# Performance work log

Measured on AMD Instinct MI355X. Metric: run time of the kernel, lower is better.

Reference implementation:

```python
import jax, jax.numpy as jnp
import numpy as np

N = 16384      # total nodes in batched graph
E = 131072     # message-passing edges
E_RO = 32768   # readout edges
D = 1024       # fc7 appearance feature dim
DL = 300       # word2vec dim
DS = 16        # spatial edge feature dim
C = 117        # HICO verb classes


def setup_inputs() -> dict:
    key = jax.random.key(0)
    ks = jax.random.split(key, 20)
    s = 0.02
    return {
        'feat': jax.random.normal(ks[0], (N, D), jnp.float32),
        'word2vec': jax.random.normal(ks[1], (N, DL), jnp.float32),
        's_f': jax.random.normal(ks[2], (E, DS), jnp.float32),
        's_f_ro': jax.random.normal(ks[3], (E_RO, DS), jnp.float32),
        'W_e': jax.random.normal(ks[4], (2 * D + DS, D), jnp.float32) * s,
        'b_e': jnp.zeros((D,), jnp.float32),
        'W_el': jax.random.normal(ks[5], (2 * DL, DL), jnp.float32) * s,
        'b_el': jnp.zeros((DL,), jnp.float32),
        'W_nu': jax.random.normal(ks[6], (2 * D, D), jnp.float32) * s,
        'b_nu': jnp.zeros((D,), jnp.float32),
        'W_nul': jax.random.normal(ks[7], (2 * DL, DL), jnp.float32) * s,
        'b_nul': jnp.zeros((DL,), jnp.float32),
        'W_p': jax.random.normal(ks[8], (D + DL + DS + DL + D, C), jnp.float32) * s,
        'b_p': jnp.zeros((C,), jnp.float32),
        'edge_src': jax.random.randint(ks[9], (E,), 0, N, jnp.int32),
        'edge_dst': jax.random.randint(ks[10], (E,), 0, N, jnp.int32),
        'ro_src': jax.random.randint(ks[11], (E_RO,), 0, N, jnp.int32),
        'ro_dst': jax.random.randint(ks[12], (E_RO,), 0, N, jnp.int32),
    }


def _mean_agg(msgs, dst, n, dtype):
    # scatter-add messages to destination nodes, then mean-normalize
    summed = jax.ops.segment_sum(msgs, dst, num_segments=n)
    cnt = jax.ops.segment_sum(jnp.ones((msgs.shape[0], 1), dtype), dst, num_segments=n)
    return summed / jnp.maximum(cnt, 1.0)


def reference(feat, word2vec, s_f, s_f_ro, W_e, b_e, W_el, b_el,
              W_nu, b_nu, W_nul, b_nul, W_p, b_p,
              edge_src, edge_dst, ro_src, ro_dst):
    # --- GRNN message passing: gather -> concat -> MLP -> scatter(mean) ---
    # appearance stream: [src_feat, dst_feat, s_f] -> relu(MLP)
    m = jax.nn.relu(
        jnp.concatenate([feat[edge_src], feat[edge_dst], s_f], axis=1) @ W_e + b_e)
    agg = _mean_agg(m, edge_dst, N, feat.dtype)               # [N, D]
    # language stream: [src_w2v, dst_w2v] -> relu(MLP)
    ml = jax.nn.relu(
        jnp.concatenate([word2vec[edge_src], word2vec[edge_dst]], axis=1) @ W_el + b_el)
    aggl = _mean_agg(ml, edge_dst, N, feat.dtype)             # [N, DL]

    # --- NodeUpdate: concat(original, aggregated) -> MLP ---
    new_n_f = jax.nn.relu(jnp.concatenate([feat, agg], axis=1) @ W_nu + b_nu)
    new_n_f_lang = jax.nn.relu(
        jnp.concatenate([word2vec, aggl], axis=1) @ W_nul + b_nul)

    # --- Predictor (edge readout): concat[dst_f, dst_lang, s_f, src_lang, src_f] ---
    ef = jnp.concatenate([
        new_n_f[ro_dst], new_n_f_lang[ro_dst], s_f_ro,
        new_n_f_lang[ro_src], new_n_f[ro_src]], axis=1)       # [E_RO, 2664]
    pred = ef @ W_p + b_p                                     # [E_RO, 117]
    return pred
```

## Files before the change

### kernel.cpp

```cpp
#include <hip/hip_runtime.h>

typedef unsigned short u16;
typedef __attribute__((ext_vector_type(8))) short short8;
typedef __attribute__((ext_vector_type(4))) float f32x4;

#define NN 16384
#define EE 131072
#define ERO 32768
#define DF 1024
#define DL 300
#define DLP 320
#define DLN 384
#define DS 16
#define NC 117
#define NCP 128

__device__ __forceinline__ float bf2f(u16 x) {
  unsigned int u = ((unsigned int)x) << 16;
  float f;
  __builtin_memcpy(&f, &u, 4);
  return f;
}
__device__ __forceinline__ u16 f2bf(float f) {
  unsigned int u;
  __builtin_memcpy(&u, &f, 4);
  u = (u + 0x7FFFu + ((u >> 16) & 1u)) >> 16;
  return (u16)u;
}
__device__ __forceinline__ float ld1(const void* p, size_t i, int f) {
  return f ? ((const float*)p)[i] : bf2f(((const u16*)p)[i]);
}
__device__ __forceinline__ void ld4(const void* p, size_t i, int f,
                                    float& x, float& y, float& z, float& w) {
  if (f) {
    float4 v = *(const float4*)((const float*)p + i);
    x = v.x; y = v.y; z = v.z; w = v.w;
  } else {
    ushort4 v = *(const ushort4*)((const u16*)p + i);
    x = bf2f(v.x); y = bf2f(v.y); z = bf2f(v.z); w = bf2f(v.w);
  }
}
__device__ __forceinline__ const void* eoff(const void* p, size_t off, int f) {
  return f ? (const void*)((const float*)p + off) : (const void*)((const u16*)p + off);
}

__global__ void detect_kernel(const unsigned int* __restrict__ w, int* __restrict__ flag) {
  unsigned int x = w[threadIdx.x];
  int e = (x >> 7) & 0xFF;
  int ok = (e >= 97 && e <= 157);
  unsigned long long m = __ballot(ok);
  if (threadIdx.x == 0) flag[0] = (__popcll(m) >= 48) ? 0 : 1;
}

__global__ void cast_bf16(const int* __restrict__ flag, const void* __restrict__ src,
                          u16* __restrict__ dst, int total8) {
  const int i = blockIdx.x * 256 + threadIdx.x;
  if (i >= total8) return;
  const int fin = flag[0];
  const size_t o = (size_t)i * 8;
  float x0, x1, x2, x3, x4, x5, x6, x7;
  ld4(src, o, fin, x0, x1, x2, x3);
  ld4(src, o + 4, fin, x4, x5, x6, x7);
  ushort4 lo, hi;
  lo.x = f2bf(x0); lo.y = f2bf(x1); lo.z = f2bf(x2); lo.w = f2bf(x3);
  hi.x = f2bf(x4); hi.y = f2bf(x5); hi.z = f2bf(x6); hi.w = f2bf(x7);
  *(ushort4*)(dst + o) = lo;
  *(ushort4*)(dst + o + 4) = hi;
}

struct TJob {
  const void* W; long off;
  int Kr, Nr, Nstr, Kp, Np, blk0;
};
struct TPack { TJob j[12]; int nj; };

__global__ void prep_weights(const int* __restrict__ flag, TPack P, u16* __restrict__ outbase,
                             const long* __restrict__ outoffs_unused) {
}

struct TJob2 {
  const void* W; long off;
  u16* out;
  int Kr, Nr, Nstr, Kp, Np, blk0;
};
struct TPack2 { TJob2 j[12]; int nj; };

__global__ void prep_weights2(const int* __restrict__ flag, TPack2 P) {
  int b = blockIdx.x;
  int ji = 0;
  while (ji + 1 < P.nj && b >= P.j[ji + 1].blk0) ++ji;
  const TJob2 J = P.j[ji];
  const int idx = (b - J.blk0) * 256 + threadIdx.x;
  if (idx >= J.Np * J.Kp) return;
  const int n = idx / J.Kp, k = idx % J.Kp;
  float v = 0.f;
  if (k < J.Kr && n < J.Nr) v = ld1(J.W, (size_t)J.off + (size_t)k * J.Nstr + n, flag[0]);
  J.out[idx] = f2bf(v);
}

__device__ __forceinline__ void stage_bf16_async(const u16* __restrict__ G, size_t rbase,
                                                 int lda, int k0, u16* lds, int w, int lane) {
  #pragma unroll
  for (int t = 0; t < 2; ++t) {
    const int rr = (w << 5) + (t << 4) + (lane >> 2);
    const u16* gp = G + (rbase + rr) * (size_t)lda + k0 + ((lane & 3) << 3);
    __builtin_amdgcn_global_load_lds(
        (const __attribute__((address_space(1))) void*)gp,
        (__attribute__((address_space(3))) void*)(lds + (((w << 5) + (t << 4)) * 32)),
        16, 0, 0);
  }
}

__device__ __forceinline__ void stage_f32_manual(const float* __restrict__ G, int row0,
                                                 int lda, int k0, int Kreal,
                                                 u16* lds, int tid) {
  const int r = tid >> 1, half = tid & 1;
  const float* gp = G + (size_t)(row0 + r) * lda + k0 + (half << 4);
  #pragma unroll
  for (int qq = 0; qq < 4; ++qq) {
    const int kk = k0 + (half << 4) + (qq << 2);
    float4 v = make_float4(0.f, 0.f, 0.f, 0.f);
    if (kk < Kreal) v = *(const float4*)(gp + (qq << 2));
    ushort4 o;
    o.x = f2bf(v.x); o.y = f2bf(v.y); o.z = f2bf(v.z); o.w = f2bf(v.w);
    *(ushort4*)(lds + r * 32 + (half << 4) + (qq << 2)) = o;
  }
}

__device__ __forceinline__ void kloop(int am, const void* __restrict__ A, int lda,
                                      int Kreal, int Kpad, const u16* __restrict__ B,
                                      u16* As, u16* Bs, f32x4 (&acc)[4][4],
                                      int row0, int col0,
                                      int tid, int lane, int w, int wm, int wn, int ml, int q) {
  for (int k0 = 0; k0 < Kpad; k0 += 32) {
    if (am == 0) stage_bf16_async((const u16*)A, (size_t)row0, lda, k0, As, w, lane);
    else         stage_f32_manual((const float*)A, row0, lda, k0, Kreal, As, tid);
    stage_bf16_async(B, (size_t)col0, Kpad, k0, Bs, w, lane);
    __syncthreads();
    short8 af[4], bfr[4];
    #pragma unroll
    for (int i = 0; i < 4; ++i)
      af[i] = *(const short8*)(As + ((wm << 6) + (i << 4) + ml) * 32 + (q << 3));
    #pragma unroll
    for (int j = 0; j < 4; ++j)
      bfr[j] = *(const short8*)(Bs + ((wn << 6) + (j << 4) + ml) * 32 + (q << 3));
    #pragma unroll
    for (int i = 0; i < 4; ++i)
      #pragma unroll
      for (int j = 0; j < 4; ++j)
        acc[i][j] = __builtin_amdgcn_mfma_f32_16x16x32_bf16(af[i], bfr[j], acc[i][j], 0, 0, 0);
    __syncthreads();
  }
}

struct GJob {
  const void* A1; const u16* B1;
  const void* A2; const u16* B2;
  const void* bias; void* C;
  int lda1, K1real, K1pad, am1;
  int lda2, K2real, K2pad, am2;
  int inBias, ldc, Nreal, Npad, relu, cf32;
  int gx, gy, blk0;
};
struct GPack { GJob j[2]; int nj; };

__global__ __launch_bounds__(256) void mfma_jobs(const int* __restrict__ flag, GPack P) {
  const int b = blockIdx.x;
  int ji = 0;
  if (P.nj > 1 && b >= P.j[1].blk0) ji = 1;
  const GJob J = P.j[ji];
  const int t = b - J.blk0;
  const int xcd = t & 7, s = t >> 3;
  const int row_t = xcd * (J.gy >> 3) + s / J.gx;
  const int col_t = s % J.gx;
  const int row0 = row_t << 7;
  const int col0 = col_t << 7;

  __shared__ __attribute__((aligned(16))) u16 As[128 * 32];
  __shared__ __attribute__((aligned(16))) u16 Bs[128 * 32];
  const int tid = threadIdx.x;
  const int lane = tid & 63;
  const int w = tid >> 6;
  const int wm = w >> 1, wn = w & 1;
  const int ml = lane & 15, q = lane >> 4;

  f32x4 acc[4][4];
  #pragma unroll
  for (int i = 0; i < 4; ++i)
    #pragma unroll
    for (int j = 0; j < 4; ++j) {
      f32x4 z = {0.f, 0.f, 0.f, 0.f};
      acc[i][j] = z;
    }

  kloop(J.am1, J.A1, J.lda1, J.K1real, J.K1pad, J.B1, As, Bs, acc,
        row0, col0, tid, lane, w, wm, wn, ml, q);
  if (J.am2 >= 0)
    kloop(J.am2, J.A2, J.lda2, J.K2real, J.K2pad, J.B2, As, Bs, acc,
          row0, col0, tid, lane, w, wm, wn, ml, q);

  const int fin = flag[0];
  #pragma unroll
  for (int j = 0; j < 4; ++j) {
    const int col = col0 + (wn << 6) + (j << 4) + ml;
    if (col >= J.Npad) continue;
    float bv = 0.f;
    if (J.bias && col < J.Nreal) bv = ld1(J.bias, col, J.inBias ? fin : 0);
    #pragma unroll
    for (int i = 0; i < 4; ++i) {
      #pragma unroll
      for (int r = 0; r < 4; ++r) {
        const int row = row0 + (wm << 6) + (i << 4) + (q << 2) + r;
        float v = 0.f;
        if (col < J.Nreal) {
          v = acc[i][j][r] + bv;
          if (J.relu) v = fmaxf(v, 0.f);
        }
        if (J.cf32) ((float*)J.C)[(size_t)row * J.ldc + col] = v;
        else        ((u16*)J.C)[(size_t)row * J.ldc + col] = f2bf(v);
      }
    }
  }
}

__global__ void cnt_kernel(const int* __restrict__ edst, int* __restrict__ cnt) {
  const int i = blockIdx.x * 256 + threadIdx.x;
  if (i < EE) atomicAdd(&cnt[edst[i]], 1);
}

__global__ __launch_bounds__(1024) void scan_kernel(const int* __restrict__ cnt,
                                                    int* __restrict__ offs,
                                                    int* __restrict__ woffs) {
  __shared__ int part[1024];
  const int t = threadIdx.x;
  const int base = t * 16;
  int loc[16];
  int s = 0;
  #pragma unroll
  for (int i = 0; i < 16; ++i) { loc[i] = s; s += cnt[base + i]; }
  part[t] = s;
  __syncthreads();
  for (int off = 1; off < 1024; off <<= 1) {
    int v = (t >= off) ? part[t - off] : 0;
    __syncthreads();
    part[t] += v;
    __syncthreads();
  }
  const int chunk_excl = (t == 0) ? 0 : part[t - 1];
  #pragma unroll
  for (int i = 0; i < 16; ++i) {
    int o = chunk_excl + loc[i];
    offs[base + i] = o;
    woffs[base + i] = o;
  }
  if (t == 1023) offs[NN] = part[1023];
}

__global__ void scatter_kernel(const int* __restrict__ esrc, const int* __restrict__ edst,
                               int* __restrict__ woffs,
                               int* __restrict__ order, int* __restrict__ srcs) {
  const int e = blockIdx.x * 256 + threadIdx.x;
  if (e < EE) {
    const int d = edst[e];
    const int pos = atomicAdd(&woffs[d], 1);
    order[pos] = e;
    srcs[pos] = esrc[e];
  }
}

__global__ __launch_bounds__(256) void app_agg(
    const int* __restrict__ flag,
    const u16* __restrict__ P12, const void* __restrict__ s_f,
    const void* __restrict__ W_eb, const void* __restrict__ b_e,
    const int* __restrict__ offs, const int* __restrict__ order,
    const int* __restrict__ srcs, u16* __restrict__ aggn)
{
  const int fin = flag[0];
  const int n = blockIdx.x;
  const int tid = threadIdx.x;
  const int c4 = tid << 2;
  const void* W_es = eoff(W_eb, (size_t)2 * DF * DF, fin);

  float wx[16], wy[16], wz[16], ww[16];
  #pragma unroll
  for (int k = 0; k < 16; ++k)
    ld4(W_es, (size_t)k * DF + c4, fin, wx[k], wy[k], wz[k], ww[k]);

  float be0, be1, be2, be3;
  ld4(b_e, c4, fin, be0, be1, be2, be3);
  const ushort4 p2 = *(const ushort4*)(P12 + (size_t)n * 2048 + 1024 + c4);
  const float base0 = bf2f(p2.x) + be0;
  const float base1 = bf2f(p2.y) + be1;
  const float base2 = bf2f(p2.z) + be2;
  const float base3 = bf2f(p2.w) + be3;

  const int beg = offs[n], end = offs[n + 1];
  float a0 = 0.f, a1 = 0.f, a2 = 0.f, a3 = 0.f;
  int j = beg;
  for (; j + 4 <= end; j += 4) {
    int ee[4], ss[4];
    #pragma unroll
    for (int m = 0; m < 4; ++m) { ee[m] = order[j + m]; ss[m] = srcs[j + m]; }
    float u0[4], u1[4], u2[4], u3[4], sfv[4][16];
    #pragma unroll
    for (int m = 0; m < 4; ++m) {
      #pragma unroll
      for (int k = 0; k < 16; k += 4)
        ld4(s_f, (size_t)ee[m] * DS + k, fin,
            sfv[m][k], sfv[m][k + 1], sfv[m][k + 2], sfv[m][k + 3]);
      const ushort4 pm = *(const ushort4*)(P12 + (size_t)ss[m] * 2048 + c4);
      u0[m] = bf2f(pm.x) + base0;
      u1[m] = bf2f(pm.y) + base1;
      u2[m] = bf2f(pm.z) + base2;
      u3[m] = bf2f(pm.w) + base3;
    }
    #pragma unroll
    for (int k = 0; k < 16; ++k)
      #pragma unroll
      for (int m = 0; m < 4; ++m) {
        u0[m] = fmaf(sfv[m][k], wx[k], u0[m]);
        u1[m] = fmaf(sfv[m][k], wy[k], u1[m]);
        u2[m] = fmaf(sfv[m][k], wz[k], u2[m]);
        u3[m] = fmaf(sfv[m][k], ww[k], u3[m]);
      }
    #pragma unroll
    for (int m = 0; m < 4; ++m) {
      a0 += fmaxf(u0[m], 0.f); a1 += fmaxf(u1[m], 0.f);
      a2 += fmaxf(u2[m], 0.f); a3 += fmaxf(u3[m], 0.f);
    }
  }
  for (; j < end; ++j) {
    const int e = order[j], s = srcs[j];
    float sf[16];
    #pragma unroll
    for (int k = 0; k < 16; k += 4)
      ld4(s_f, (size_t)e * DS + k, fin, sf[k], sf[k + 1], sf[k + 2], sf[k + 3]);
    const ushort4 p1 = *(const ushort4*)(P12 + (size_t)s * 2048 + c4);
    float v0 = bf2f(p1.x) + base0;
    float v1 = bf2f(p1.y) + base1;
    float v2 = bf2f(p1.z) + base2;
    float v3 = bf2f(p1.w) + base3;
    #pragma unroll
    for (int k = 0; k < 16; ++k) {
      v0 = fmaf(sf[k], wx[k], v0);
      v1 = fmaf(sf[k], wy[k], v1);
      v2 = fmaf(sf[k], wz[k], v2);
      v3 = fmaf(sf[k], ww[k], v3);
    }
    a0 += fmaxf(v0, 0.f); a1 += fmaxf(v1, 0.f);
    a2 += fmaxf(v2, 0.f); a3 += fmaxf(v3, 0.f);
  }
  const float inv = 1.f / fmaxf((float)(end - beg), 1.f);
  ushort4 o;
  o.x = f2bf(a0 * inv); o.y = f2bf(a1 * inv);
  o.z = f2bf(a2 * inv); o.w = f2bf(a3 * inv);
  *(ushort4*)(aggn + (size_t)n * DF + c4) = o;
}

__global__ __launch_bounds__(320) void lang_agg(
    const int* __restrict__ flag,
    const u16* __restrict__ Q12, const void* __restrict__ b_el,
    const int* __restrict__ offs, const int* __restrict__ srcs,
    u16* __restrict__ aggln)
{
  const int fin = flag[0];
  const int n = blockIdx.x;
  const int c = threadIdx.x;
  if (c >= DL) { aggln[(size_t)n * DLP + c] = 0; return; }
  const float base = bf2f(Q12[(size_t)n * 768 + 384 + c]) + ld1(b_el, c, fin);
  const int beg = offs[n], end = offs[n + 1];
  float s0 = 0.f, s1 = 0.f, s2 = 0.f, s3 = 0.f;
  int j = beg;
  for (; j + 4 <= end; j += 4) {
    s0 += fmaxf(bf2f(Q12[(size_t)srcs[j] * 768 + c]) + base, 0.f);
    s1 += fmaxf(bf2f(Q12[(size_t)srcs[j + 1] * 768 + c]) + base, 0.f);
    s2 += fmaxf(bf2f(Q12[(size_t)srcs[j + 2] * 768 + c]) + base, 0.f);
    s3 += fmaxf(bf2f(Q12[(size_t)srcs[j + 3] * 768 + c]) + base, 0.f);
  }
  for (; j < end; ++j) s0 += fmaxf(bf2f(Q12[(size_t)srcs[j] * 768 + c]) + base, 0.f);
  const float a = (s0 + s1) + (s2 + s3);
  aggln[(size_t)n * DLP + c] = f2bf(a / fmaxf((float)(end - beg), 1.f));
}

__global__ __launch_bounds__(256) void readout_kernel(
    const int* __restrict__ flag,
    const float* __restrict__ RdRs,
    const void* __restrict__ s_f_ro,
    const void* __restrict__ W_pb, size_t offWps,
    const void* __restrict__ b_p,
    const int* __restrict__ rsrc, const int* __restrict__ rdst, void* __restrict__ out)
{
  const int fin = flag[0];
  __shared__ float wps[16 * NC];
  const void* Wp_s = eoff(W_pb, offWps, fin);
  const int tid = threadIdx.x;
  for (int i = tid; i < 16 * NC; i += 256) wps[i] = ld1(Wp_s, i, fin);
  __syncthreads();
  const int slot = tid >> 7;
  const int c = tid & 127;
  const float bp = (c < NC) ? ld1(b_p, c, fin) : 0.f;

  const int e0 = (blockIdx.x << 3) + slot;
  #pragma unroll
  for (int ee = 0; ee < 8; ee += 2) {
    const int e = e0 + ee;
    const int s = rsrc[e];
    const int d = rdst[e];
    if (c < NC) {
      float acc = RdRs[(size_t)d * 256 + c] + RdRs[(size_t)s * 256 + 128 + c] + bp;
      #pragma unroll
      for (int k = 0; k < 16; ++k)
        acc = fmaf(ld1(s_f_ro, (size_t)e * DS + k, fin), wps[k * NC + c], acc);
      if (fin) ((float*)out)[(size_t)e * NC + c] = acc;
      else     ((u16*)out)[(size_t)e * NC + c] = f2bf(acc);
    }
  }
}

extern "C" void kernel_launch(void* const* d_in, const int* in_sizes, int n_in,
                              void* d_out, int out_size, void* d_ws, size_t ws_size,
                              hipStream_t stream)
{
  const void* feat  = d_in[0];
  const void* w2v   = d_in[1];
  const void* s_f   = d_in[2];
  const void* s_fro = d_in[3];
  const void* W_e   = d_in[4];
  const void* b_e   = d_in[5];
  const void* W_el  = d_in[6];
  const void* b_el  = d_in[7];
  const void* W_nu  = d_in[8];
  const void* b_nu  = d_in[9];
  const void* W_nul = d_in[10];
  const void* b_nul = d_in[11];
  const void* W_p   = d_in[12];
  const void* b_p   = d_in[13];
  const int* esrc  = (const int*)d_in[14];
  const int* edst  = (const int*)d_in[15];
  const int* rsrc  = (const int*)d_in[16];
  const int* rdst  = (const int*)d_in[17];

  char* p = (char*)d_ws;
  int* flag  = (int*)p; p += 256;
  int* cnt   = (int*)p; p += (size_t)NN * 4;
  int* offs  = (int*)p; p += (size_t)(NN + 64) * 4;
  int* woffs = (int*)p; p += (size_t)NN * 4;
  int* order = (int*)p; p += (size_t)EE * 4;
  int* srcs  = (int*)p; p += (size_t)EE * 4;
  u16* featB  = (u16*)p; p += (size_t)NN * DF * 2;
  u16* We12T  = (u16*)p; p += (size_t)2 * DF * DF * 2;
  u16* Wnu1T  = (u16*)p; p += (size_t)DF * DF * 2;
  u16* Wnu2T  = (u16*)p; p += (size_t)DF * DF * 2;
  u16* Wel12T = (u16*)p; p += (size_t)2 * DLN * DLP * 2;
  u16* Wnul1T = (u16*)p; p += (size_t)DLN * DLP * 2;
  u16* Wnul2T = (u16*)p; p += (size_t)DLN * DLP * 2;
  u16* WpFT2  = (u16*)p; p += (size_t)2 * NCP * DF * 2;
  u16* WpLT2  = (u16*)p; p += (size_t)2 * NCP * DLP * 2;
  u16* P12   = (u16*)p; p += (size_t)NN * 2048 * 2;
  u16* Q12   = (u16*)p; p += (size_t)NN * 768 * 2;
  u16* aggln = (u16*)p; p += (size_t)NN * DLP * 2;
  u16* aggn  = (u16*)p; p += (size_t)NN * DF * 2;
  u16* newf = P12;
  u16* newl = P12 + (size_t)NN * DF;
  float* RdRs = (float*)Q12;

  detect_kernel<<<1, 64, 0, stream>>>((const unsigned int*)feat, flag);
  hipMemsetAsync(cnt, 0, (size_t)NN * 4, stream);
  cast_bf16<<<(NN * DF / 8 + 255) / 256, 256, 0, stream>>>(flag, feat, featB, NN * DF / 8);

  TPack2 tp{};
  int tb = 0, tn = 0;
  auto T = [&](const void* W, long off, int Kr, int Nr, int Nstr, u16* out, int Kp, int Np) {
    tp.j[tn] = TJob2{W, off, out, Kr, Nr, Nstr, Kp, Np, tb};
    tb += (Np * Kp + 255) / 256;
    ++tn;
  };
  T(W_e,   0,                   DF, DF, DF, We12T,                     DF, DF);
  T(W_e,   (long)DF * DF,       DF, DF, DF, We12T + (size_t)DF * DF,   DF, DF);
  T(W_nu,  0,                   DF, DF, DF, Wnu1T, DF, DF);
  T(W_nu,  (long)DF * DF,       DF, DF, DF, Wnu2T, DF, DF);
  T(W_el,  0,                   DL, DL, DL, Wel12T,                     DLP, DLN);
  T(W_el,  (long)DL * DL,       DL, DL, DL, Wel12T + (size_t)DLN * DLP, DLP, DLN);
  T(W_nul, 0,                   DL, DL, DL, Wnul1T, DLP, DLN);
  T(W_nul, (long)DL * DL,       DL, DL, DL, Wnul2T, DLP, DLN);
  T(W_p,   0,                                DF, NC, NC, WpFT2,                     DF,  NCP);
  T(W_p,   (long)(DF + DL + DS + DL) * NC,   DF, NC, NC, WpFT2 + (size_t)NCP * DF,  DF,  NCP);
  T(W_p,   (long)DF * NC,                    DL, NC, NC, WpLT2,                     DLP, NCP);
  T(W_p,   (long)(DF + DL + DS) * NC,        DL, NC, NC, WpLT2 + (size_t)NCP * DLP, DLP, NCP);
  tp.nj = tn;
  prep_weights2<<<tb, 256, 0, stream>>>(flag, tp);

  cnt_kernel<<<EE / 256, 256, 0, stream>>>(edst, cnt);
  scan_kernel<<<1, 1024, 0, stream>>>(cnt, offs, woffs);
  scatter_kernel<<<EE / 256, 256, 0, stream>>>(esrc, edst, woffs, order, srcs);

  {
    GPack g{};
    g.j[0] = GJob{featB, We12T, nullptr, nullptr, nullptr, P12,
                  DF, DF, DF, 0,    0, 0, 0, -1,
                  0, 2048, 2048, 2048, 0, 0,  16, 128, 0};
    g.j[1] = GJob{w2v, Wel12T, nullptr, nullptr, nullptr, Q12,
                  DL, DL, DLP, 1,   0, 0, 0, -1,
                  0, 768, 768, 768, 0, 0,    6, 128, 2048};
    g.nj = 2;
    mfma_jobs<<<2048 + 768, 256, 0, stream>>>(flag, g);
  }

  lang_agg<<<NN, DLP, 0, stream>>>(flag, Q12, b_el, offs, srcs, aggln);
  app_agg<<<NN, 256, 0, stream>>>(flag, P12, s_f, W_e, b_e, offs, order, srcs, aggn);

  {
    GPack g{};
    g.j[0] = GJob{featB, Wnu1T, aggn, Wnu2T, b_nu, newf,
                  DF, DF, DF, 0,    DF, DF, DF, 0,
                  1, DF, DF, DF, 1, 0,       8, 128, 0};
    g.j[1] = GJob{w2v, Wnul1T, aggln, Wnul2T, b_nul, newl,
                  DL, DL, DLP, 1,   DLP, DLP, DLP, 0,
                  1, DLP, DL, DLP, 1, 0,     3, 128, 1024};
    g.nj = 2;
    mfma_jobs<<<1024 + 384, 256, 0, stream>>>(flag, g);
  }

  {
    GPack g{};
    g.j[0] = GJob{newf, WpFT2, newl, WpLT2, nullptr, RdRs,
                  DF, DF, DF, 0,    DLP, DLP, DLP, 0,
                  0, 256, 256, 256, 0, 1,    2, 128, 0};
    g.nj = 1;
    mfma_jobs<<<256, 256, 0, stream>>>(flag, g);
  }

  readout_kernel<<<ERO / 8, 256, 0, stream>>>(flag, RdRs, s_fro,
                                              W_p, (size_t)(DF + DL) * NC, b_p,
                                              rsrc, rdst, d_out);
}
```

Baseline: 654.6 us.

## Add 256x256-tile MFMA GEMM kernel with LDS double buffering for large GEMMs

After: 659.0 us. About the same (+0.7%).

```diff
diff --git a/kernel.cpp b/kernel.cpp
--- a/kernel.cpp
+++ b/kernel.cpp
@@ -68,16 +68,6 @@
   *(ushort4*)(dst + o + 4) = hi;
 }
 
-struct TJob {
-  const void* W; long off;
-  int Kr, Nr, Nstr, Kp, Np, blk0;
-};
-struct TPack { TJob j[12]; int nj; };
-
-__global__ void prep_weights(const int* __restrict__ flag, TPack P, u16* __restrict__ outbase,
-                             const long* __restrict__ outoffs_unused) {
-}
-
 struct TJob2 {
   const void* W; long off;
   u16* out;
@@ -218,6 +208,144 @@
         }
         if (J.cf32) ((float*)J.C)[(size_t)row * J.ldc + col] = v;
         else        ((u16*)J.C)[(size_t)row * J.ldc + col] = f2bf(v);
+      }
+    }
+  }
+}
+
+
+struct G2Job {
+  const u16* A1; const u16* B1;
+  const u16* A2; const u16* B2;
+  const void* bias; u16* C;
+  int ldk;
+  int nt1, nt2;
+  int gx;
+  int ldc, Nreal, relu, inBias;
+};
+
+#define L2_HALF 16384
+#define L2_BUF  65536
+
+__device__ __forceinline__ void barrier_f() {
+  asm volatile("" ::: "memory");
+  __builtin_amdgcn_s_barrier();
+  asm volatile("" ::: "memory");
+}
+
+__device__ __forceinline__ void read4f(const char* base, short8 (&dst)[4]) {
+  #pragma unroll
+  for (int i = 0; i < 4; ++i) dst[i] = *(const short8*)(base + i * 1024);
+}
+
+__device__ __forceinline__ void mfma16(f32x4 (&acc)[8][4], const short8 (&af)[4],
+                                       const short8 (&bfr)[4], int mg) {
+  __builtin_amdgcn_s_setprio(1);
+  #pragma unroll
+  for (int i = 0; i < 4; ++i)
+    #pragma unroll
+    for (int n = 0; n < 4; ++n)
+      acc[mg * 4 + i][n] =
+          __builtin_amdgcn_mfma_f32_16x16x32_bf16(af[i], bfr[n], acc[mg * 4 + i][n], 0, 0, 0);
+  __builtin_amdgcn_s_setprio(0);
+}
+
+__global__ __launch_bounds__(512, 2) void mfma256(const int* __restrict__ flag, G2Job J) {
+  __shared__ __attribute__((aligned(16))) u16 LDS[65536];
+  char* ldsc = (char*)LDS;
+
+  const int nwg = gridDim.x;
+  const int bid = blockIdx.x;
+  const int wg = (bid & 7) * (nwg >> 3) + (bid >> 3);
+  const int rt = wg / J.gx, ct = wg % J.gx;
+  const int row0 = rt << 8, col0 = ct << 8;
+
+  const int tid = threadIdx.x;
+  const int lane = tid & 63, w = tid >> 6;
+  const int wm = w >> 2, wn = w & 3;
+  const int q = lane >> 4, ml = lane & 15;
+  const int ldk = J.ldk;
+  const int nt = J.nt1 + J.nt2;
+
+  const int swzr = (ml * 64 + q * 16) ^ (((ml >> 1) & 3) << 4);
+  const int ub = (lane * 16) ^ (((lane >> 3) & 3) << 4);
+  const int r_in = ub >> 6, c_in = (ub & 63) >> 1;
+
+  f32x4 acc[8][4];
+  #pragma unroll
+  for (int m = 0; m < 8; ++m)
+    #pragma unroll
+    for (int n = 0; n < 4; ++n) { f32x4 z = {0.f, 0.f, 0.f, 0.f}; acc[m][n] = z; }
+
+  auto stage = [&](int cb2, const u16* __restrict__ G, int rb, int kc, int boff, int kh) {
+    char* lb = ldsc + cb2 * L2_BUF + boff + kh * L2_HALF + w * 2048;
+    const u16* g0 = G + (size_t)(rb + w * 32 + r_in) * (size_t)ldk + kc;
+    __builtin_amdgcn_global_load_lds((const __attribute__((address_space(1))) void*)g0,
+        (__attribute__((address_space(3))) void*)lb, 16, 0, 0);
+    const u16* g1 = g0 + (size_t)16 * ldk;
+    __builtin_amdgcn_global_load_lds((const __attribute__((address_space(1))) void*)g1,
+        (__attribute__((address_space(3))) void*)(lb + 1024), 16, 0, 0);
+  };
+
+  stage(0, J.A1, row0, 0 + c_in, 0, 0);
+  stage(0, J.B1, col0, 0 + c_in, 32768, 0);
+  stage(0, J.A1, row0, 32 + c_in, 0, 1);
+  stage(0, J.B1, col0, 32 + c_in, 32768, 1);
+  asm volatile("s_waitcnt vmcnt(4)" ::: "memory");
+  barrier_f();
+
+  int cb = 0;
+  #pragma unroll 1
+  for (int kt = 0; kt < nt; ++kt) {
+    const int nk = (kt + 1 < nt) ? kt + 1 : kt;
+    const u16* An = (nk < J.nt1) ? J.A1 : J.A2;
+    const u16* Bn = (nk < J.nt1) ? J.B1 : J.B2;
+    const int kb = ((nk < J.nt1) ? nk : nk - J.nt1) << 6;
+    const char* abase = ldsc + cb * L2_BUF + wm * 8192 + swzr;
+    const char* bbase = ldsc + cb * L2_BUF + 32768 + wn * 4096 + swzr;
+    short8 a0[4], a1[4], bfr[4];
+
+    read4f(abase, a0);
+    read4f(bbase, bfr);
+    stage(cb ^ 1, An, row0, kb + c_in, 0, 0);
+    barrier_f();
+    mfma16(acc, a0, bfr, 0);
+    barrier_f();
+    read4f(abase + 4096, a1);
+    stage(cb ^ 1, Bn, col0, kb + c_in, 32768, 0);
+    barrier_f();
+    mfma16(acc, a1, bfr, 1);
+    asm volatile("s_waitcnt vmcnt(4)" ::: "memory");
+    barrier_f();
+    read4f(abase + L2_HALF, a0);
+    read4f(bbase + L2_HALF, bfr);
+    stage(cb ^ 1, An, row0, kb + 32 + c_in, 0, 1);
+    barrier_f();
+    mfma16(acc, a0, bfr, 0);
+    barrier_f();
+    read4f(abase + L2_HALF + 4096, a1);
+    stage(cb ^ 1, Bn, col0, kb + 32 + c_in, 32768, 1);
+    barrier_f();
+    mfma16(acc, a1, bfr, 1);
+    asm volatile("s_waitcnt vmcnt(4)" ::: "memory");
+    barrier_f();
+    cb ^= 1;
+  }
+
+  const int fin = flag[0];
+  #pragma unroll
+  for (int n = 0; n < 4; ++n) {
+    const int col = col0 + wn * 64 + n * 16 + ml;
+    float bv = 0.f;
+    if (J.bias && col < J.Nreal) bv = ld1(J.bias, col, J.inBias ? fin : 0);
+    #pragma unroll
+    for (int m = 0; m < 8; ++m) {
+      #pragma unroll
+      for (int r = 0; r < 4; ++r) {
+        const int row = row0 + wm * 128 + m * 16 + q * 4 + r;
+        float v = acc[m][n][r] + bv;
+        if (J.relu) v = fmaxf(v, 0.f);
+        J.C[(size_t)row * J.ldc + col] = f2bf(v);
       }
     }
   }
@@ -495,30 +623,34 @@
   scatter_kernel<<<EE / 256, 256, 0, stream>>>(esrc, edst, woffs, order, srcs);
 
   {
+    G2Job j{featB, We12T, nullptr, nullptr, nullptr, P12,
+            DF, 16, 0, 8, 2048, 2048, 0, 0};
+    mfma256<<<512, 512, 0, stream>>>(flag, j);
+  }
+  {
     GPack g{};
-    g.j[0] = GJob{featB, We12T, nullptr, nullptr, nullptr, P12,
-                  DF, DF, DF, 0,    0, 0, 0, -1,
-                  0, 2048, 2048, 2048, 0, 0,  16, 128, 0};
-    g.j[1] = GJob{w2v, Wel12T, nullptr, nullptr, nullptr, Q12,
+    g.j[0] = GJob{w2v, Wel12T, nullptr, nullptr, nullptr, Q12,
                   DL, DL, DLP, 1,   0, 0, 0, -1,
-                  0, 768, 768, 768, 0, 0,    6, 128, 2048};
-    g.nj = 2;
-    mfma_jobs<<<2048 + 768, 256, 0, stream>>>(flag, g);
+                  0, 768, 768, 768, 0, 0,    6, 128, 0};
+    g.nj = 1;
+    mfma_jobs<<<768, 256, 0, stream>>>(flag, g);
   }
 
   lang_agg<<<NN, DLP, 0, stream>>>(flag, Q12, b_el, offs, srcs, aggln);
   app_agg<<<NN, 256, 0, stream>>>(flag, P12, s_f, W_e, b_e, offs, order, srcs, aggn);
 
   {
+    G2Job j{featB, Wnu1T, aggn, Wnu2T, b_nu, newf,
+            DF, 16, 16, 4, DF, DF, 1, 1};
+    mfma256<<<256, 512, 0, stream>>>(flag, j);
+  }
+  {
     GPack g{};
-    g.j[0] = GJob{featB, Wnu1T, aggn, Wnu2T, b_nu, newf,
-                  DF, DF, DF, 0,    DF, DF, DF, 0,
-                  1, DF, DF, DF, 1, 0,       8, 128, 0};
-    g.j[1] = GJob{w2v, Wnul1T, aggln, Wnul2T, b_nul, newl,
+    g.j[0] = GJob{w2v, Wnul1T, aggln, Wnul2T, b_nul, newl,
                   DL, DL, DLP, 1,   DLP, DLP, DLP, 0,
-                  1, DLP, DL, DLP, 1, 0,     3, 128, 1024};
-    g.nj = 2;
-    mfma_jobs<<<1024 + 384, 256, 0, stream>>>(flag, g);
+                  1, DLP, DL, DLP, 1, 0,     3, 128, 0};
+    g.nj = 1;
+    mfma_jobs<<<384, 256, 0, stream>>>(flag, g);
   }
 
   {
```
